# Performance work log

Hardware: AMD Instinct MI355X
Metric: run time of the kernel (lower is better)

Reference implementation:

```python
import jax, jax.numpy as jnp
import numpy as np

IN, HID, OUT = 64, 256, 64
B, NSTEPS, DELAY = 256, 1024, 20


def setup_inputs() -> dict:
    key = jax.random.key(0)
    ks = jax.random.split(key, 8)
    s = 0.05
    return {
        "input": jax.random.normal(ks[0], (B, NSTEPS, IN), jnp.float32),
        "W_ih_x": jax.random.normal(ks[1], (4 * HID, IN), jnp.float32) * s,
        "W_ih_fb": jax.random.normal(ks[2], (4 * HID, OUT), jnp.float32) * s,
        "W_hh": jax.random.normal(ks[3], (4 * HID, HID), jnp.float32) * s,
        "b_ih": jax.random.normal(ks[4], (4 * HID,), jnp.float32) * s,
        "b_hh": jax.random.normal(ks[5], (4 * HID,), jnp.float32) * s,
        "W_out": jax.random.normal(ks[6], (OUT, HID), jnp.float32) * s,
        "b_out": jax.random.normal(ks[7], (OUT,), jnp.float32) * s,
        "delay": DELAY,
    }


def reference(input, W_ih_x, W_ih_fb, W_hh, b_ih, b_hh, W_out, b_out, delay):
    b, nsteps, _ = input.shape
    H = W_hh.shape[1]
    O = W_out.shape[0]
    # Precompute the input contribution to the gates for all timesteps:
    # gates_t = x_t @ W_ih_x.T + fb @ W_ih_fb.T + h @ W_hh.T + b_ih + b_hh
    xg = jnp.einsum("btd,gd->tbg", input, W_ih_x) + (b_ih + b_hh)  # [T, B, 4H]

    h0 = jnp.zeros((b, H), input.dtype)
    c0 = jnp.zeros((b, H), input.dtype)
    buf0 = jnp.zeros((delay, b, O), input.dtype)  # ring buffer of past outputs
    ptr0 = jnp.zeros((), jnp.int32)

    def step(carry, xg_t):
        h, c, buf, ptr = carry
        fb = buf[ptr]  # output from `delay` steps ago (zeros initially)
        gates = xg_t + fb @ W_ih_fb.T + h @ W_hh.T  # [B, 4H]
        i, f, g, o = jnp.split(gates, 4, axis=-1)  # torch LSTMCell gate order
        c = jax.nn.sigmoid(f) * c + jax.nn.sigmoid(i) * jnp.tanh(g)
        h = jax.nn.sigmoid(o) * jnp.tanh(c)
        out = h @ W_out.T + b_out  # [B, O]
        buf = buf.at[ptr].set(out)
        ptr = (ptr + 1) % delay
        return (h, c, buf, ptr), out

    _, outs = jax.lax.scan(step, (h0, c0, buf0, ptr0), xg)  # outs: [T, B, O]
    return jnp.transpose(outs, (1, 0, 2))  # [B, T, O]
```

## Files before the change

kernel.cpp:

```cpp
#include <hip/hip_runtime.h>


#define BATCH   256
#define TSTEPS  1024
#define IN_DIM  64
#define HID     256
#define G4      1024
#define OUT_DIM 64
#define DELAY   20
#define CH      8
#define NCH     (TSTEPS / CH)
#define NTHR    512
#define REGP    22

typedef unsigned int u32;
typedef _Float16 half2_t __attribute__((ext_vector_type(2)));

union H2U { u32 u; half2_t h; };
union H1U { unsigned short s; _Float16 h; };

__device__ __forceinline__ u32 pack2(float a, float b) {
    H2U x; x.h = half2_t{(_Float16)a, (_Float16)b}; return x.u;
}
__device__ __forceinline__ unsigned short f16bits(float a) {
    H1U x; x.h = (_Float16)a; return x.s;
}
__device__ __forceinline__ float lo16(u32 u) {
    H1U x; x.s = (unsigned short)(u & 0xffffu); return (float)x.h;
}
__device__ __forceinline__ float hi16(u32 u) {
    H1U x; x.s = (unsigned short)(u >> 16); return (float)x.h;
}
__device__ __forceinline__ float dot2(u32 w, u32 h, float acc) {
    H2U a; a.u = w; H2U b; b.u = h;
    return __builtin_amdgcn_fdot2(a.h, b.h, acc, false);
}
__device__ __forceinline__ float sigm(float x) {
    float e = __expf(-fabsf(x));
    float p = 1.f / (1.f + e);
    return x >= 0.f ? p : 1.f - p;
}
__device__ __forceinline__ float tanh_f(float x) {
    float e = __expf(-2.f * fabsf(x));
    float r = (1.f - e) / (1.f + e);
    return x >= 0.f ? r : -r;
}

#define OFF_LDSW  0
#define OFF_CB    98304
#define OFF_PART  114688
#define OFF_HH    122880
#define OFF_RING  123904
#define OFF_XF    126464
#define SMEM_BYTES 128640

#define WS_BPK    0
#define WS_WGR    262144
#define WS_WOUT   327680
#define WS_BSUM   360448
#define WS_HG     364544
#define WS_NEED   (364544 + 2097152)

__device__ __forceinline__ int orig_row(int gp) {
    return (gp & 3) * 256 + (gp >> 2);
}

__global__ void prepack(const float* __restrict__ Wx,
                        const float* __restrict__ Wfb,
                        const float* __restrict__ Whh,
                        const float* __restrict__ Wout,
                        const float* __restrict__ bih,
                        const float* __restrict__ bhh,
                        uint4* __restrict__ Bpk4,
                        uint4* __restrict__ WgR4,
                        u32* __restrict__ Woutpk,
                        float* __restrict__ bsum_g)
{
    int id = blockIdx.x * 256 + threadIdx.x;
    if (id < 16384) {
        int t = id & 511, rest = id >> 9;
        int kb = rest & 15, j = rest >> 4;
        int r = orig_row(2 * t + j);
        int k0 = kb * 8;
        const float* src = (k0 < 64) ? (Wx + (size_t)r * 64 + k0)
                                     : (Wfb + (size_t)r * 64 + (k0 - 64));
        uint4 v;
        v.x = pack2(src[0], src[1]); v.y = pack2(src[2], src[3]);
        v.z = pack2(src[4], src[5]); v.w = pack2(src[6], src[7]);
        Bpk4[id] = v;
    } else if (id < 16384 + 4096) {
        int s = id - 16384;
        int tt = s & 511, q = s >> 9;
        int kq = tt >> 7, gl = tt & 127;
        int r = orig_row(gl * 8 + q);
        const float* w = Whh + (size_t)r * HID + kq * 64 + 56;
        uint4 v;
        v.x = pack2(w[0], w[1]); v.y = pack2(w[2], w[3]);
        v.z = pack2(w[4], w[5]); v.w = pack2(w[6], w[7]);
        WgR4[s] = v;
    } else if (id < 16384 + 4096 + 8192) {
        int s = id - 20480;
        int c = s & 3, o = (s >> 2) & 63, w4 = s >> 8;
        int kp = w4 * 4 + c;
        Woutpk[s] = pack2(Wout[o * HID + 2 * kp], Wout[o * HID + 2 * kp + 1]);
    } else if (id < 16384 + 4096 + 8192 + 1024) {
        int g = id - 28672;
        int r = orig_row(g);
        bsum_g[g] = bih[r] + bhh[r];
    }
}

__global__ __attribute__((amdgpu_flat_work_group_size(NTHR, NTHR)))
__attribute__((amdgpu_waves_per_eu(2, 2)))
void lstm_persist(const float* __restrict__ input,
                  const float* __restrict__ Whh,
                  const float* __restrict__ bout_g,
                  const uint4* __restrict__ Bpk4,
                  const uint4* __restrict__ WgR4,
                  const u32* __restrict__ Woutpk,
                  const float* __restrict__ bsum_g,
                  unsigned short* __restrict__ hg_all,
                  float* __restrict__ out)
{
    extern __shared__ char smem[];
    uint2*          ldsw  = (uint2*)(smem + OFF_LDSW);
    u32*            cb32  = (u32*)(smem + OFF_CB);
    unsigned short* part  = (unsigned short*)(smem + OFF_PART);
    unsigned short* hh    = (unsigned short*)(smem + OFF_HH);
    unsigned short* ring  = (unsigned short*)(smem + OFF_RING);
    u32*            xfst  = (u32*)(smem + OFF_XF);

    const int tid = threadIdx.x;
    const int b   = blockIdx.x;
    const int kq  = tid >> 7;
    const int gl  = tid & 127;

    const float* xin  = input + (size_t)b * TSTEPS * IN_DIM;
    float*       outp = out + (size_t)b * TSTEPS * OUT_DIM;
    unsigned short* hg = hg_all + (size_t)b * (16 * HID);
    const float bo_reg = bout_g[tid & 63];

    u32 wreg[8][REGP];
#pragma unroll
    for (int q = 0; q < 8; ++q) {
        const int r = orig_row(gl * 8 + q);
        const float* wrow = Whh + (size_t)r * HID + kq * 64;
#pragma unroll
        for (int p = 0; p < REGP; ++p) {
            float2 w2 = *(const float2*)(wrow + 2 * p);
            wreg[q][p] = pack2(w2.x, w2.y);
        }
#pragma unroll
        for (int j = 0; j < 3; ++j) {
            float2 wa = *(const float2*)(wrow + 44 + 4 * j);
            float2 wb = *(const float2*)(wrow + 46 + 4 * j);
            uint2 tv;
            tv.x = pack2(wa.x, wa.y);
            tv.y = pack2(wb.x, wb.y);
            ldsw[j * 4096 + q * 512 + tid] = tv;
        }
    }
#pragma unroll
    for (int q = 0; q < 8; ++q)
#pragma unroll
        for (int p = 0; p < REGP; ++p)
            asm volatile("" : "+v"(wreg[q][p]));

    if (tid < 256) { hh[tid] = 0; hh[256 + tid] = 0; }
    __syncthreads();

    float c_state = 0.f;

    auto out_chunk = [&](int tbase) {
        const int lt = tid >> 6, o = tid & 63;
        const int t = tbase + lt;
        const uint4* hrow = (const uint4*)(hg + (t & 15) * HID);
        const uint4* wp = (const uint4*)Woutpk;
        float a = bo_reg;
        for (int w4 = 0; w4 < 32; ++w4) {
            uint4 wv = wp[w4 * 64 + o];
            uint4 hv = hrow[w4];
            a = dot2(wv.x, hv.x, a); a = dot2(wv.y, hv.y, a);
            a = dot2(wv.z, hv.z, a); a = dot2(wv.w, hv.w, a);
        }
        outp[(size_t)t * OUT_DIM + o] = a;
        ring[(t % DELAY) * 64 + o] = f16bits(a);
    };

#pragma unroll 1
    for (int ch = 0; ch < NCH; ++ch) {
        const int t0 = ch * CH;
        if (ch > 0) out_chunk(t0 - CH);
        __syncthreads();

        {
            int row = tid >> 6, p = tid & 63;
            int t = t0 + row;
            u32 v;
            if (p < 32) {
                float2 x2 = *(const float2*)(xin + (size_t)t * IN_DIM + 2 * p);
                v = pack2(x2.x, x2.y);
            } else {
                int src = t - DELAY;
                if (src >= 0) {
                    int d = 2 * (p - 32);
                    int sl = src % DELAY;
                    v = (u32)ring[sl * 64 + d] | ((u32)ring[sl * 64 + d + 1] << 16);
                } else v = 0u;
            }
            xfst[row * 68 + p] = v;
        }
        __syncthreads();

        {
            float accA[8], accB[8];
#pragma unroll
            for (int i = 0; i < 8; ++i) { accA[i] = 0.f; accB[i] = 0.f; }
            const uint4* bA = Bpk4 + tid;
            const uint4* bB = Bpk4 + 16 * 512 + tid;
#pragma unroll 1
            for (int kb = 0; kb < 16; ++kb) {
                uint4 wA = bA[kb * 512];
                uint4 wB = bB[kb * 512];
#pragma unroll
                for (int tl = 0; tl < 8; ++tl) {
                    uint4 xv = *(const uint4*)(xfst + tl * 68 + kb * 4);
                    accA[tl] = dot2(wA.x, xv.x, accA[tl]);
                    accA[tl] = dot2(wA.y, xv.y, accA[tl]);
                    accA[tl] = dot2(wA.z, xv.z, accA[tl]);
                    accA[tl] = dot2(wA.w, xv.w, accA[tl]);
                    accB[tl] = dot2(wB.x, xv.x, accB[tl]);
                    accB[tl] = dot2(wB.y, xv.y, accB[tl]);
                    accB[tl] = dot2(wB.z, xv.z, accB[tl]);
                    accB[tl] = dot2(wB.w, xv.w, accB[tl]);
                }
            }
            float2 bs = *(const float2*)(bsum_g + 2 * tid);
#pragma unroll
            for (int tl = 0; tl < 8; ++tl)
                cb32[tl * 512 + tid] = pack2(accA[tl] + bs.x, accB[tl] + bs.y);
        }
        __syncthreads();

#pragma unroll 1
        for (int tl = 0; tl < CH; ++tl) {
            const int t = t0 + tl;
            const u32* hrow = (const u32*)hh + ((t + 1) & 1) * 128 + kq * 32;

            float acc[8];
            if (kq == 0) {
                uint4 cv = *(const uint4*)(cb32 + tl * 512 + gl * 4);
                acc[0] = lo16(cv.x); acc[1] = hi16(cv.x);
                acc[2] = lo16(cv.y); acc[3] = hi16(cv.y);
                acc[4] = lo16(cv.z); acc[5] = hi16(cv.z);
                acc[6] = lo16(cv.w); acc[7] = hi16(cv.w);
            } else {
#pragma unroll
                for (int q = 0; q < 8; ++q) acc[q] = 0.f;
            }
            {
                uint4 h0 = *(const uint4*)(hrow + 0);
                uint4 h1 = *(const uint4*)(hrow + 4);
                uint4 h2 = *(const uint4*)(hrow + 8);
                uint4 h3 = *(const uint4*)(hrow + 12);
#pragma unroll
                for (int q = 0; q < 8; ++q) {
                    acc[q] = dot2(wreg[q][0],  h0.x, acc[q]);
                    acc[q] = dot2(wreg[q][1],  h0.y, acc[q]);
                    acc[q] = dot2(wreg[q][2],  h0.z, acc[q]);
                    acc[q] = dot2(wreg[q][3],  h0.w, acc[q]);
                    acc[q] = dot2(wreg[q][4],  h1.x, acc[q]);
                    acc[q] = dot2(wreg[q][5],  h1.y, acc[q]);
                    acc[q] = dot2(wreg[q][6],  h1.z, acc[q]);
                    acc[q] = dot2(wreg[q][7],  h1.w, acc[q]);
                    acc[q] = dot2(wreg[q][8],  h2.x, acc[q]);
                    acc[q] = dot2(wreg[q][9],  h2.y, acc[q]);
                    acc[q] = dot2(wreg[q][10], h2.z, acc[q]);
                    acc[q] = dot2(wreg[q][11], h2.w, acc[q]);
                    acc[q] = dot2(wreg[q][12], h3.x, acc[q]);
                    acc[q] = dot2(wreg[q][13], h3.y, acc[q]);
                    acc[q] = dot2(wreg[q][14], h3.z, acc[q]);
                    acc[q] = dot2(wreg[q][15], h3.w, acc[q]);
                }
            }
            {
                uint4 h4 = *(const uint4*)(hrow + 16);
                uint4 h5 = *(const uint4*)(hrow + 20);
                uint4 h6 = *(const uint4*)(hrow + 24);
                uint4 h7 = *(const uint4*)(hrow + 28);
#pragma unroll
                for (int grp = 0; grp < 2; ++grp) {
                    const uint4* wgp = WgR4 + (grp * 4) * 512 + tid;
                    uint4 wg0 = wgp[0];
                    uint4 wg1 = wgp[512];
                    uint4 wg2 = wgp[1024];
                    uint4 wg3 = wgp[1536];
#pragma unroll
                    for (int j = 0; j < 4; ++j) {
                        const int q = grp * 4 + j;
                        acc[q] = dot2(wreg[q][16], h4.x, acc[q]);
                        acc[q] = dot2(wreg[q][17], h4.y, acc[q]);
                        acc[q] = dot2(wreg[q][18], h4.z, acc[q]);
                        acc[q] = dot2(wreg[q][19], h4.w, acc[q]);
                        acc[q] = dot2(wreg[q][20], h5.x, acc[q]);
                        acc[q] = dot2(wreg[q][21], h5.y, acc[q]);
                        uint2 lw0 = ldsw[0 * 4096 + q * 512 + tid];
                        uint2 lw1 = ldsw[1 * 4096 + q * 512 + tid];
                        uint2 lw2 = ldsw[2 * 4096 + q * 512 + tid];
                        acc[q] = dot2(lw0.x, h5.z, acc[q]);
                        acc[q] = dot2(lw0.y, h5.w, acc[q]);
                        acc[q] = dot2(lw1.x, h6.x, acc[q]);
                        acc[q] = dot2(lw1.y, h6.y, acc[q]);
                        acc[q] = dot2(lw2.x, h6.z, acc[q]);
                        acc[q] = dot2(lw2.y, h6.w, acc[q]);
                        uint4 wg = (j == 0) ? wg0 : (j == 1) ? wg1 : (j == 2) ? wg2 : wg3;
                        acc[q] = dot2(wg.x, h7.x, acc[q]);
                        acc[q] = dot2(wg.y, h7.y, acc[q]);
                        acc[q] = dot2(wg.z, h7.z, acc[q]);
                        acc[q] = dot2(wg.w, h7.w, acc[q]);
                    }
                }
            }
            {
                uint4 pw;
                pw.x = pack2(acc[0], acc[1]); pw.y = pack2(acc[2], acc[3]);
                pw.z = pack2(acc[4], acc[5]); pw.w = pack2(acc[6], acc[7]);
                *(uint4*)(part + kq * G4 + gl * 8) = pw;
            }
            __syncthreads();

            if (tid < 256) {
                float s0 = 0.f, s1 = 0.f, s2 = 0.f, s3 = 0.f;
#pragma unroll
                for (int k = 0; k < 4; ++k) {
                    uint2 rd = *(const uint2*)(part + k * G4 + tid * 4);
                    s0 += lo16(rd.x); s1 += hi16(rd.x);
                    s2 += lo16(rd.y); s3 += hi16(rd.y);
                }
                c_state = sigm(s1) * c_state + sigm(s0) * tanh_f(s2);
                float hval = sigm(s3) * tanh_f(c_state);
                unsigned short hb = f16bits(hval);
                hh[(t & 1) * HID + tid] = hb;
                hg[(t & 15) * HID + tid] = hb;
            }
            __syncthreads();
        }
    }
    out_chunk(TSTEPS - CH);
}

extern "C" void kernel_launch(void* const* d_in, const int* in_sizes, int n_in,
                              void* d_out, int out_size, void* d_ws, size_t ws_size,
                              hipStream_t stream)
{
    (void)in_sizes; (void)n_in; (void)out_size;
    const float* input = (const float*)d_in[0];
    const float* Wx    = (const float*)d_in[1];
    const float* Wfb   = (const float*)d_in[2];
    const float* Whh   = (const float*)d_in[3];
    const float* bih   = (const float*)d_in[4];
    const float* bhh   = (const float*)d_in[5];
    const float* Wo    = (const float*)d_in[6];
    const float* bog   = (const float*)d_in[7];
    float* out = (float*)d_out;

    if (ws_size < (size_t)WS_NEED) return;

    static bool attr_set = false;
    if (!attr_set) {
        hipFuncSetAttribute((const void*)lstm_persist,
                            hipFuncAttributeMaxDynamicSharedMemorySize,
                            SMEM_BYTES);
        attr_set = true;
    }

    uint4* Bpk4   = (uint4*)((char*)d_ws + WS_BPK);
    uint4* WgR4   = (uint4*)((char*)d_ws + WS_WGR);
    u32*   Woutpk = (u32*)((char*)d_ws + WS_WOUT);
    float* bsum_g = (float*)((char*)d_ws + WS_BSUM);
    unsigned short* hg = (unsigned short*)((char*)d_ws + WS_HG);

    prepack<<<dim3(116), dim3(256), 0, stream>>>(
        Wx, Wfb, Whh, Wo, bih, bhh, Bpk4, WgR4, Woutpk, bsum_g);
    lstm_persist<<<dim3(BATCH), dim3(NTHR), SMEM_BYTES, stream>>>(
        input, Whh, bog, Bpk4, WgR4, Woutpk, bsum_g, hg, out);
}
```

Baseline: 5.114 ms.

## Double block to 1024 threads splitting recurrent K into eight slices

Raises the workgroup from 512 to 1024 threads and splits the hidden-to-gate reduction into eight 32-wide K slices instead of four 64-wide ones. Each thread now keeps 8 packed weights per gate row in registers, with the rest coming from LDS and global (L2) streams. The h history moves from global workspace into shared memory, and the input projection gives one gate per thread. The aim is to shorten the serial per-step dot-product chain. The cost is a larger partial-sum reduction, more global weight loads per step and higher LDS use.

```diff
diff --git a/kernel.cpp b/kernel.cpp
--- a/kernel.cpp
+++ b/kernel.cpp
@@ -5,13 +5,11 @@
 #define TSTEPS  1024
 #define IN_DIM  64
 #define HID     256
-#define G4      1024
 #define OUT_DIM 64
 #define DELAY   20
 #define CH      8
 #define NCH     (TSTEPS / CH)
-#define NTHR    512
-#define REGP    22
+#define NTHR    1024
 
 typedef unsigned int u32;
 typedef _Float16 half2_t __attribute__((ext_vector_type(2)));
@@ -46,20 +44,21 @@
     return x >= 0.f ? r : -r;
 }
 
-#define OFF_LDSW  0
+#define OFF_LDSWA 0
+#define OFF_LDSWB 65536
 #define OFF_CB    98304
 #define OFF_PART  114688
-#define OFF_HH    122880
-#define OFF_RING  123904
-#define OFF_XF    126464
-#define SMEM_BYTES 128640
-
-#define WS_BPK    0
-#define WS_WGR    262144
-#define WS_WOUT   327680
-#define WS_BSUM   360448
-#define WS_HG     364544
-#define WS_NEED   (364544 + 2097152)
+#define OFF_RING  131072
+#define OFF_XF    133632
+#define OFF_HG    135808
+#define SMEM_BYTES 144000
+
+#define WS_BPK   0
+#define WS_WGSA  262144
+#define WS_WGSB  393216
+#define WS_WOUT  425984
+#define WS_BSUM  458752
+#define WS_NEED  462848
 
 __device__ __forceinline__ int orig_row(int gp) {
     return (gp & 3) * 256 + (gp >> 2);
@@ -72,7 +71,8 @@
                         const float* __restrict__ bih,
                         const float* __restrict__ bhh,
                         uint4* __restrict__ Bpk4,
-                        uint4* __restrict__ WgR4,
+                        uint4* __restrict__ WgSA4,
+                        uint4* __restrict__ WgSB4,
                         u32* __restrict__ Woutpk,
                         float* __restrict__ bsum_g)
 {
@@ -88,103 +88,134 @@
         v.x = pack2(src[0], src[1]); v.y = pack2(src[2], src[3]);
         v.z = pack2(src[4], src[5]); v.w = pack2(src[6], src[7]);
         Bpk4[id] = v;
-    } else if (id < 16384 + 4096) {
+    } else if (id < 24576) {
         int s = id - 16384;
-        int tt = s & 511, q = s >> 9;
-        int kq = tt >> 7, gl = tt & 127;
+        int t = s & 1023, q = s >> 10;
+        int ke = t >> 7, gl = t & 127;
         int r = orig_row(gl * 8 + q);
-        const float* w = Whh + (size_t)r * HID + kq * 64 + 56;
+        const float* w = Whh + (size_t)r * HID + ke * 32 + 22;
         uint4 v;
         v.x = pack2(w[0], w[1]); v.y = pack2(w[2], w[3]);
         v.z = pack2(w[4], w[5]); v.w = pack2(w[6], w[7]);
-        WgR4[s] = v;
-    } else if (id < 16384 + 4096 + 8192) {
-        int s = id - 20480;
+        WgSA4[s] = v;
+    } else if (id < 26624) {
+        int s = id - 24576;
+        int t = s & 1023, qz = s >> 10;
+        int ke = t >> 7, gl = t & 127;
+        u32 c[4];
+#pragma unroll
+        for (int j = 0; j < 4; ++j) {
+            int r = orig_row(gl * 8 + qz * 4 + j);
+            const float* w = Whh + (size_t)r * HID + ke * 32 + 30;
+            c[j] = pack2(w[0], w[1]);
+        }
+        uint4 v; v.x = c[0]; v.y = c[1]; v.z = c[2]; v.w = c[3];
+        WgSB4[s] = v;
+    } else if (id < 34816) {
+        int s = id - 26624;
         int c = s & 3, o = (s >> 2) & 63, w4 = s >> 8;
         int kp = w4 * 4 + c;
         Woutpk[s] = pack2(Wout[o * HID + 2 * kp], Wout[o * HID + 2 * kp + 1]);
-    } else if (id < 16384 + 4096 + 8192 + 1024) {
-        int g = id - 28672;
+    } else if (id < 35840) {
+        int g = id - 34816;
         int r = orig_row(g);
         bsum_g[g] = bih[r] + bhh[r];
     }
 }
 
 __global__ __attribute__((amdgpu_flat_work_group_size(NTHR, NTHR)))
-__attribute__((amdgpu_waves_per_eu(2, 2)))
 void lstm_persist(const float* __restrict__ input,
                   const float* __restrict__ Whh,
                   const float* __restrict__ bout_g,
                   const uint4* __restrict__ Bpk4,
-                  const uint4* __restrict__ WgR4,
+                  const uint4* __restrict__ WgSA4,
+                  const uint4* __restrict__ WgSB4,
                   const u32* __restrict__ Woutpk,
                   const float* __restrict__ bsum_g,
-                  unsigned short* __restrict__ hg_all,
                   float* __restrict__ out)
 {
     extern __shared__ char smem[];
-    uint2*          ldsw  = (uint2*)(smem + OFF_LDSW);
-    u32*            cb32  = (u32*)(smem + OFF_CB);
+    uint4*          ldswA = (uint4*)(smem + OFF_LDSWA);
+    uint4*          ldswB = (uint4*)(smem + OFF_LDSWB);
+    unsigned short* cbh   = (unsigned short*)(smem + OFF_CB);
     unsigned short* part  = (unsigned short*)(smem + OFF_PART);
-    unsigned short* hh    = (unsigned short*)(smem + OFF_HH);
     unsigned short* ring  = (unsigned short*)(smem + OFF_RING);
     u32*            xfst  = (u32*)(smem + OFF_XF);
+    unsigned short* hgs   = (unsigned short*)(smem + OFF_HG);
 
     const int tid = threadIdx.x;
     const int b   = blockIdx.x;
-    const int kq  = tid >> 7;
+    const int ke  = tid >> 7;
     const int gl  = tid & 127;
 
     const float* xin  = input + (size_t)b * TSTEPS * IN_DIM;
     float*       outp = out + (size_t)b * TSTEPS * OUT_DIM;
-    unsigned short* hg = hg_all + (size_t)b * (16 * HID);
     const float bo_reg = bout_g[tid & 63];
 
-    u32 wreg[8][REGP];
+    u32 wreg[8][8];
 #pragma unroll
     for (int q = 0; q < 8; ++q) {
         const int r = orig_row(gl * 8 + q);
-        const float* wrow = Whh + (size_t)r * HID + kq * 64;
-#pragma unroll
-        for (int p = 0; p < REGP; ++p) {
+        const float* wrow = Whh + (size_t)r * HID + ke * 32;
+#pragma unroll
+        for (int p = 0; p < 8; ++p) {
             float2 w2 = *(const float2*)(wrow + 2 * p);
             wreg[q][p] = pack2(w2.x, w2.y);
         }
-#pragma unroll
-        for (int j = 0; j < 3; ++j) {
-            float2 wa = *(const float2*)(wrow + 44 + 4 * j);
-            float2 wb = *(const float2*)(wrow + 46 + 4 * j);
-            uint2 tv;
-            tv.x = pack2(wa.x, wa.y);
-            tv.y = pack2(wb.x, wb.y);
-            ldsw[j * 4096 + q * 512 + tid] = tv;
-        }
+    }
+#pragma unroll
+    for (int qq = 0; qq < 4; ++qq) {
+        const int r0 = orig_row(gl * 8 + 2 * qq);
+        const int r1 = orig_row(gl * 8 + 2 * qq + 1);
+        const float* w0 = Whh + (size_t)r0 * HID + ke * 32 + 16;
+        const float* w1 = Whh + (size_t)r1 * HID + ke * 32 + 16;
+        uint4 v;
+        v.x = pack2(w0[0], w0[1]); v.y = pack2(w0[2], w0[3]);
+        v.z = pack2(w1[0], w1[1]); v.w = pack2(w1[2], w1[3]);
+        ldswA[qq * 1024 + tid] = v;
+    }
+#pragma unroll
+    for (int qz = 0; qz < 2; ++qz) {
+        u32 c[4];
+#pragma unroll
+        for (int j = 0; j < 4; ++j) {
+            const int r = orig_row(gl * 8 + qz * 4 + j);
+            const float* w = Whh + (size_t)r * HID + ke * 32 + 20;
+            c[j] = pack2(w[0], w[1]);
+        }
+        uint4 v; v.x = c[0]; v.y = c[1]; v.z = c[2]; v.w = c[3];
+        ldswB[qz * 1024 + tid] = v;
     }
 #pragma unroll
     for (int q = 0; q < 8; ++q)
 #pragma unroll
-        for (int p = 0; p < REGP; ++p)
+        for (int p = 0; p < 8; ++p)
             asm volatile("" : "+v"(wreg[q][p]));
 
-    if (tid < 256) { hh[tid] = 0; hh[256 + tid] = 0; }
+    {
+        u32* hz = (u32*)hgs;
+        hz[tid] = 0u; hz[1024 + tid] = 0u;
+    }
     __syncthreads();
 
     float c_state = 0.f;
 
     auto out_chunk = [&](int tbase) {
-        const int lt = tid >> 6, o = tid & 63;
-        const int t = tbase + lt;
-        const uint4* hrow = (const uint4*)(hg + (t & 15) * HID);
-        const uint4* wp = (const uint4*)Woutpk;
-        float a = bo_reg;
-        for (int w4 = 0; w4 < 32; ++w4) {
-            uint4 wv = wp[w4 * 64 + o];
-            uint4 hv = hrow[w4];
-            a = dot2(wv.x, hv.x, a); a = dot2(wv.y, hv.y, a);
-            a = dot2(wv.z, hv.z, a); a = dot2(wv.w, hv.w, a);
-        }
-        outp[(size_t)t * OUT_DIM + o] = a;
-        ring[(t % DELAY) * 64 + o] = f16bits(a);
+        if (tid < 512) {
+            const int lt = tid >> 6, o = tid & 63;
+            const int t = tbase + lt;
+            const uint4* hrow = (const uint4*)(hgs + (t & 15) * HID);
+            const uint4* wp = (const uint4*)Woutpk;
+            float a = bo_reg;
+            for (int w4 = 0; w4 < 32; ++w4) {
+                uint4 wv = wp[w4 * 64 + o];
+                uint4 hv = hrow[w4];
+                a = dot2(wv.x, hv.x, a); a = dot2(wv.y, hv.y, a);
+                a = dot2(wv.z, hv.z, a); a = dot2(wv.w, hv.w, a);
+            }
+            outp[(size_t)t * OUT_DIM + o] = a;
+            ring[(t % DELAY) * 64 + o] = f16bits(a);
+        }
     };
 
 #pragma unroll 1
@@ -193,7 +224,7 @@
         if (ch > 0) out_chunk(t0 - CH);
         __syncthreads();
 
-        {
+        if (tid < 512) {
             int row = tid >> 6, p = tid & 63;
             int t = t0 + row;
             u32 v;
@@ -213,43 +244,44 @@
         __syncthreads();
 
         {
-            float accA[8], accB[8];
-#pragma unroll
-            for (int i = 0; i < 8; ++i) { accA[i] = 0.f; accB[i] = 0.f; }
-            const uint4* bA = Bpk4 + tid;
-            const uint4* bB = Bpk4 + 16 * 512 + tid;
+            float acc8[8];
+#pragma unroll
+            for (int i = 0; i < 8; ++i) acc8[i] = 0.f;
+            const uint4* bA = Bpk4 + (tid & 1) * (16 * 512) + (tid >> 1);
 #pragma unroll 1
             for (int kb = 0; kb < 16; ++kb) {
-                uint4 wA = bA[kb * 512];
-                uint4 wB = bB[kb * 512];
+                uint4 w = bA[kb * 512];
 #pragma unroll
                 for (int tl = 0; tl < 8; ++tl) {
                     uint4 xv = *(const uint4*)(xfst + tl * 68 + kb * 4);
-                    accA[tl] = dot2(wA.x, xv.x, accA[tl]);
-                    accA[tl] = dot2(wA.y, xv.y, accA[tl]);
-                    accA[tl] = dot2(wA.z, xv.z, accA[tl]);
-                    accA[tl] = dot2(wA.w, xv.w, accA[tl]);
-                    accB[tl] = dot2(wB.x, xv.x, accB[tl]);
-                    accB[tl] = dot2(wB.y, xv.y, accB[tl]);
-                    accB[tl] = dot2(wB.z, xv.z, accB[tl]);
-                    accB[tl] = dot2(wB.w, xv.w, accB[tl]);
+                    acc8[tl] = dot2(w.x, xv.x, acc8[tl]);
+                    acc8[tl] = dot2(w.y, xv.y, acc8[tl]);
+                    acc8[tl] = dot2(w.z, xv.z, acc8[tl]);
+                    acc8[tl] = dot2(w.w, xv.w, acc8[tl]);
                 }
             }
-            float2 bs = *(const float2*)(bsum_g + 2 * tid);
+            float bs = bsum_g[tid];
 #pragma unroll
             for (int tl = 0; tl < 8; ++tl)
-                cb32[tl * 512 + tid] = pack2(accA[tl] + bs.x, accB[tl] + bs.y);
+                cbh[tl * 1024 + tid] = f16bits(acc8[tl] + bs);
         }
         __syncthreads();
 
 #pragma unroll 1
         for (int tl = 0; tl < CH; ++tl) {
             const int t = t0 + tl;
-            const u32* hrow = (const u32*)hh + ((t + 1) & 1) * 128 + kq * 32;
+            const u32* hrow = (const u32*)hgs + ((t - 1) & 15) * 128 + ke * 16;
+
+            const uint4* wsa = WgSA4 + tid;
+            uint4 sA0 = wsa[0];
+            uint4 sA1 = wsa[1024];
+            uint4 sA2 = wsa[2048];
+            uint4 sA3 = wsa[3072];
+            uint4 sB0 = WgSB4[tid];
 
             float acc[8];
-            if (kq == 0) {
-                uint4 cv = *(const uint4*)(cb32 + tl * 512 + gl * 4);
+            if (ke == 0) {
+                uint4 cv = *(const uint4*)(cbh + tl * 1024 + gl * 8);
                 acc[0] = lo16(cv.x); acc[1] = hi16(cv.x);
                 acc[2] = lo16(cv.y); acc[3] = hi16(cv.y);
                 acc[4] = lo16(cv.z); acc[5] = hi16(cv.z);
@@ -258,90 +290,89 @@
 #pragma unroll
                 for (int q = 0; q < 8; ++q) acc[q] = 0.f;
             }
-            {
-                uint4 h0 = *(const uint4*)(hrow + 0);
-                uint4 h1 = *(const uint4*)(hrow + 4);
-                uint4 h2 = *(const uint4*)(hrow + 8);
-                uint4 h3 = *(const uint4*)(hrow + 12);
-#pragma unroll
-                for (int q = 0; q < 8; ++q) {
-                    acc[q] = dot2(wreg[q][0],  h0.x, acc[q]);
-                    acc[q] = dot2(wreg[q][1],  h0.y, acc[q]);
-                    acc[q] = dot2(wreg[q][2],  h0.z, acc[q]);
-                    acc[q] = dot2(wreg[q][3],  h0.w, acc[q]);
-                    acc[q] = dot2(wreg[q][4],  h1.x, acc[q]);
-                    acc[q] = dot2(wreg[q][5],  h1.y, acc[q]);
-                    acc[q] = dot2(wreg[q][6],  h1.z, acc[q]);
-                    acc[q] = dot2(wreg[q][7],  h1.w, acc[q]);
-                    acc[q] = dot2(wreg[q][8],  h2.x, acc[q]);
-                    acc[q] = dot2(wreg[q][9],  h2.y, acc[q]);
-                    acc[q] = dot2(wreg[q][10], h2.z, acc[q]);
-                    acc[q] = dot2(wreg[q][11], h2.w, acc[q]);
-                    acc[q] = dot2(wreg[q][12], h3.x, acc[q]);
-                    acc[q] = dot2(wreg[q][13], h3.y, acc[q]);
-                    acc[q] = dot2(wreg[q][14], h3.z, acc[q]);
-                    acc[q] = dot2(wreg[q][15], h3.w, acc[q]);
-                }
-            }
-            {
-                uint4 h4 = *(const uint4*)(hrow + 16);
-                uint4 h5 = *(const uint4*)(hrow + 20);
-                uint4 h6 = *(const uint4*)(hrow + 24);
-                uint4 h7 = *(const uint4*)(hrow + 28);
-#pragma unroll
-                for (int grp = 0; grp < 2; ++grp) {
-                    const uint4* wgp = WgR4 + (grp * 4) * 512 + tid;
-                    uint4 wg0 = wgp[0];
-                    uint4 wg1 = wgp[512];
-                    uint4 wg2 = wgp[1024];
-                    uint4 wg3 = wgp[1536];
-#pragma unroll
-                    for (int j = 0; j < 4; ++j) {
-                        const int q = grp * 4 + j;
-                        acc[q] = dot2(wreg[q][16], h4.x, acc[q]);
-                        acc[q] = dot2(wreg[q][17], h4.y, acc[q]);
-                        acc[q] = dot2(wreg[q][18], h4.z, acc[q]);
-                        acc[q] = dot2(wreg[q][19], h4.w, acc[q]);
-                        acc[q] = dot2(wreg[q][20], h5.x, acc[q]);
-                        acc[q] = dot2(wreg[q][21], h5.y, acc[q]);
-                        uint2 lw0 = ldsw[0 * 4096 + q * 512 + tid];
-                        uint2 lw1 = ldsw[1 * 4096 + q * 512 + tid];
-                        uint2 lw2 = ldsw[2 * 4096 + q * 512 + tid];
-                        acc[q] = dot2(lw0.x, h5.z, acc[q]);
-                        acc[q] = dot2(lw0.y, h5.w, acc[q]);
-                        acc[q] = dot2(lw1.x, h6.x, acc[q]);
-                        acc[q] = dot2(lw1.y, h6.y, acc[q]);
-                        acc[q] = dot2(lw2.x, h6.z, acc[q]);
-                        acc[q] = dot2(lw2.y, h6.w, acc[q]);
-                        uint4 wg = (j == 0) ? wg0 : (j == 1) ? wg1 : (j == 2) ? wg2 : wg3;
-                        acc[q] = dot2(wg.x, h7.x, acc[q]);
-                        acc[q] = dot2(wg.y, h7.y, acc[q]);
-                        acc[q] = dot2(wg.z, h7.z, acc[q]);
-                        acc[q] = dot2(wg.w, h7.w, acc[q]);
-                    }
-                }
-            }
+
+            uint4 h0 = *(const uint4*)(hrow + 0);
+            uint4 h1 = *(const uint4*)(hrow + 4);
+#pragma unroll
+            for (int q = 0; q < 8; ++q) {
+                acc[q] = dot2(wreg[q][0], h0.x, acc[q]);
+                acc[q] = dot2(wreg[q][1], h0.y, acc[q]);
+                acc[q] = dot2(wreg[q][2], h0.z, acc[q]);
+                acc[q] = dot2(wreg[q][3], h0.w, acc[q]);
+                acc[q] = dot2(wreg[q][4], h1.x, acc[q]);
+                acc[q] = dot2(wreg[q][5], h1.y, acc[q]);
+                acc[q] = dot2(wreg[q][6], h1.z, acc[q]);
+                acc[q] = dot2(wreg[q][7], h1.w, acc[q]);
+            }
+            uint4 h2 = *(const uint4*)(hrow + 8);
+            uint4 h3 = *(const uint4*)(hrow + 12);
+
+            acc[0] = dot2(sA0.x, h2.w, acc[0]); acc[0] = dot2(sA0.y, h3.x, acc[0]);
+            acc[0] = dot2(sA0.z, h3.y, acc[0]); acc[0] = dot2(sA0.w, h3.z, acc[0]);
+            acc[1] = dot2(sA1.x, h2.w, acc[1]); acc[1] = dot2(sA1.y, h3.x, acc[1]);
+            acc[1] = dot2(sA1.z, h3.y, acc[1]); acc[1] = dot2(sA1.w, h3.z, acc[1]);
+            acc[2] = dot2(sA2.x, h2.w, acc[2]); acc[2] = dot2(sA2.y, h3.x, acc[2]);
+            acc[2] = dot2(sA2.z, h3.y, acc[2]); acc[2] = dot2(sA2.w, h3.z, acc[2]);
+            acc[3] = dot2(sA3.x, h2.w, acc[3]); acc[3] = dot2(sA3.y, h3.x, acc[3]);
+            acc[3] = dot2(sA3.z, h3.y, acc[3]); acc[3] = dot2(sA3.w, h3.z, acc[3]);
+            acc[0] = dot2(sB0.x, h3.w, acc[0]); acc[1] = dot2(sB0.y, h3.w, acc[1]);
+            acc[2] = dot2(sB0.z, h3.w, acc[2]); acc[3] = dot2(sB0.w, h3.w, acc[3]);
+
+            uint4 sA4 = wsa[4096];
+            uint4 sA5 = wsa[5120];
+            uint4 sA6 = wsa[6144];
+            uint4 sA7 = wsa[7168];
+            uint4 sB1 = WgSB4[1024 + tid];
+
+            uint4 la0 = ldswA[0 * 1024 + tid];
+            uint4 la1 = ldswA[1 * 1024 + tid];
+            uint4 la2 = ldswA[2 * 1024 + tid];
+            uint4 la3 = ldswA[3 * 1024 + tid];
+            uint4 lb0 = ldswB[tid];
+            uint4 lb1 = ldswB[1024 + tid];
+            acc[0] = dot2(la0.x, h2.x, acc[0]); acc[0] = dot2(la0.y, h2.y, acc[0]);
+            acc[1] = dot2(la0.z, h2.x, acc[1]); acc[1] = dot2(la0.w, h2.y, acc[1]);
+            acc[2] = dot2(la1.x, h2.x, acc[2]); acc[2] = dot2(la1.y, h2.y, acc[2]);
+            acc[3] = dot2(la1.z, h2.x, acc[3]); acc[3] = dot2(la1.w, h2.y, acc[3]);
+            acc[4] = dot2(la2.x, h2.x, acc[4]); acc[4] = dot2(la2.y, h2.y, acc[4]);
+            acc[5] = dot2(la2.z, h2.x, acc[5]); acc[5] = dot2(la2.w, h2.y, acc[5]);
+            acc[6] = dot2(la3.x, h2.x, acc[6]); acc[6] = dot2(la3.y, h2.y, acc[6]);
+            acc[7] = dot2(la3.z, h2.x, acc[7]); acc[7] = dot2(la3.w, h2.y, acc[7]);
+            acc[0] = dot2(lb0.x, h2.z, acc[0]); acc[1] = dot2(lb0.y, h2.z, acc[1]);
+            acc[2] = dot2(lb0.z, h2.z, acc[2]); acc[3] = dot2(lb0.w, h2.z, acc[3]);
+            acc[4] = dot2(lb1.x, h2.z, acc[4]); acc[5] = dot2(lb1.y, h2.z, acc[5]);
+            acc[6] = dot2(lb1.z, h2.z, acc[6]); acc[7] = dot2(lb1.w, h2.z, acc[7]);
+
+            acc[4] = dot2(sA4.x, h2.w, acc[4]); acc[4] = dot2(sA4.y, h3.x, acc[4]);
+            acc[4] = dot2(sA4.z, h3.y, acc[4]); acc[4] = dot2(sA4.w, h3.z, acc[4]);
+            acc[5] = dot2(sA5.x, h2.w, acc[5]); acc[5] = dot2(sA5.y, h3.x, acc[5]);
+            acc[5] = dot2(sA5.z, h3.y, acc[5]); acc[5] = dot2(sA5.w, h3.z, acc[5]);
+            acc[6] = dot2(sA6.x, h2.w, acc[6]); acc[6] = dot2(sA6.y, h3.x, acc[6]);
+            acc[6] = dot2(sA6.z, h3.y, acc[6]); acc[6] = dot2(sA6.w, h3.z, acc[6]);
+            acc[7] = dot2(sA7.x, h2.w, acc[7]); acc[7] = dot2(sA7.y, h3.x, acc[7]);
+            acc[7] = dot2(sA7.z, h3.y, acc[7]); acc[7] = dot2(sA7.w, h3.z, acc[7]);
+            acc[4] = dot2(sB1.x, h3.w, acc[4]); acc[5] = dot2(sB1.y, h3.w, acc[5]);
+            acc[6] = dot2(sB1.z, h3.w, acc[6]); acc[7] = dot2(sB1.w, h3.w, acc[7]);
+
             {
                 uint4 pw;
                 pw.x = pack2(acc[0], acc[1]); pw.y = pack2(acc[2], acc[3]);
                 pw.z = pack2(acc[4], acc[5]); pw.w = pack2(acc[6], acc[7]);
-                *(uint4*)(part + kq * G4 + gl * 8) = pw;
+                *(uint4*)(part + ke * 1024 + gl * 8) = pw;
             }
             __syncthreads();
 
             if (tid < 256) {
                 float s0 = 0.f, s1 = 0.f, s2 = 0.f, s3 = 0.f;
 #pragma unroll
-                for (int k = 0; k < 4; ++k) {
-                    uint2 rd = *(const uint2*)(part + k * G4 + tid * 4);
+                for (int k8 = 0; k8 < 8; ++k8) {
+                    uint2 rd = *(const uint2*)(part + k8 * 1024 + tid * 4);
                     s0 += lo16(rd.x); s1 += hi16(rd.x);
                     s2 += lo16(rd.y); s3 += hi16(rd.y);
                 }
                 c_state = sigm(s1) * c_state + sigm(s0) * tanh_f(s2);
                 float hval = sigm(s3) * tanh_f(c_state);
-                unsigned short hb = f16bits(hval);
-                hh[(t & 1) * HID + tid] = hb;
-                hg[(t & 15) * HID + tid] = hb;
+                hgs[(t & 15) * HID + tid] = f16bits(hval);
             }
             __syncthreads();
         }
@@ -375,13 +406,13 @@
     }
 
     uint4* Bpk4   = (uint4*)((char*)d_ws + WS_BPK);
-    uint4* WgR4   = (uint4*)((char*)d_ws + WS_WGR);
+    uint4* WgSA4  = (uint4*)((char*)d_ws + WS_WGSA);
+    uint4* WgSB4  = (uint4*)((char*)d_ws + WS_WGSB);
     u32*   Woutpk = (u32*)((char*)d_ws + WS_WOUT);
     float* bsum_g = (float*)((char*)d_ws + WS_BSUM);
-    unsigned short* hg = (unsigned short*)((char*)d_ws + WS_HG);
-
-    prepack<<<dim3(116), dim3(256), 0, stream>>>(
-        Wx, Wfb, Whh, Wo, bih, bhh, Bpk4, WgR4, Woutpk, bsum_g);
+
+    prepack<<<dim3(140), dim3(256), 0, stream>>>(
+        Wx, Wfb, Whh, Wo, bih, bhh, Bpk4, WgSA4, WgSB4, Woutpk, bsum_g);
     lstm_persist<<<dim3(BATCH), dim3(NTHR), SMEM_BYTES, stream>>>(
-        input, Whh, bog, Bpk4, WgR4, Woutpk, bsum_g, hg, out);
-}
+        input, Whh, bog, Bpk4, WgSA4, WgSB4, Woutpk, bsum_g, out);
+}
```

Measured after the change: 5.920 ms. 15.8% more time.
